# Optimization experiments

Hardware: AMD Instinct MI355X
Metric: run time of the kernel (lower is better)

The kernel has to match this reference:

```python
import jax, jax.numpy as jnp
import numpy as np

N = 50000      # num nodes
E = 1_600_000  # num edges (avg degree 32)
L = 200_000    # num label edges to decode
D_IN, H1, H2 = 256, 128, 64


def setup_inputs() -> dict:
    key = jax.random.key(0)
    ks = jax.random.split(key, 20)

    def w(k, fan_in, fan_out):
        return jax.random.normal(k, (fan_in, fan_out), jnp.float32) * (1.0 / np.sqrt(fan_in))

    return {
        'x': jax.random.normal(ks[0], (N, D_IN), jnp.float32),
        'prev0': jax.random.normal(ks[1], (N, H1), jnp.float32),
        'prev1': jax.random.normal(ks[2], (N, H2), jnp.float32),
        'Wpre1': w(ks[3], D_IN, 256), 'bpre1': jnp.zeros((256,), jnp.float32),
        'Wpre2': w(ks[4], 256, 128),  'bpre2': jnp.zeros((128,), jnp.float32),
        'Wc1': w(ks[5], 128, H1),     'bc1': jnp.zeros((H1,), jnp.float32),
        'Wc2': w(ks[6], H1, H2),      'bc2': jnp.zeros((H2,), jnp.float32),
        'Wm1': w(ks[7], 2 * H1, H1),  'bm1': jnp.zeros((H1,), jnp.float32),
        'Wm2': w(ks[8], 2 * H2, H2),  'bm2': jnp.zeros((H2,), jnp.float32),
        'Wpost': w(ks[9], H2, 2),     'bpost': jnp.zeros((2,), jnp.float32),
        'edge_index': jax.random.randint(ks[10], (2, E), 0, N, jnp.int32),
        'edge_label_index': jax.random.randint(ks[11], (2, L), 0, N, jnp.int32),
    }


def _gcn_conv(h, W, b, src, dst, n):
    """PyG GCNConv: add self-loops, sym-normalize D^-1/2 (A+I) D^-1/2 (X W) + b."""
    hw = h @ W                                   # [N, out]
    deg = jax.ops.segment_sum(jnp.ones_like(src, jnp.float32), dst, num_segments=n) + 1.0
    dinv = jax.lax.rsqrt(deg)                    # [N]
    norm = dinv[src] * dinv[dst]                 # [E]
    agg = jax.ops.segment_sum(hw[src] * norm[:, None], dst, num_segments=n)
    agg = agg + hw * (dinv * dinv)[:, None]      # self-loop term
    return agg + b


def reference(x, prev0, prev1, Wpre1, bpre1, Wpre2, bpre2, Wc1, bc1, Wc2, bc2,
              Wm1, bm1, Wm2, bm2, Wpost, bpost, edge_index, edge_label_index):
    # isnap > 0 with update='mlp'; dropout p=0.0 -> identity
    src, dst = edge_index[0], edge_index[1]
    n = x.shape[0]

    h = jax.nn.relu(x @ Wpre1 + bpre1)
    h = jax.nn.relu(h @ Wpre2 + bpre2)

    h = jax.nn.relu(_gcn_conv(h, Wc1, bc1, src, dst, n))
    h = jnp.concatenate([h, prev0], axis=1) @ Wm1 + bm1   # temporal MLP update 1
    emb0 = h

    h = jax.nn.relu(_gcn_conv(h, Wc2, bc2, src, dst, n))
    h = jnp.concatenate([h, prev1], axis=1) @ Wm2 + bm2   # temporal MLP update 2
    emb1 = h

    # hadamard edge decode
    h_had = emb1[edge_label_index[0]] * emb1[edge_label_index[1]]  # [L, H2]
    pred = jnp.sum(h_had @ Wpost + bpost, axis=-1)                 # [L]
    return pred, emb0, emb1
```

## Files before the change

### kernel.cpp

```cpp
#include <hip/hip_runtime.h>
#include <hip/hip_bf16.h>


typedef unsigned short ushort_t;
typedef __attribute__((ext_vector_type(8))) short s8v;
typedef __attribute__((ext_vector_type(4))) float f4;

#define BSHIFT 8

__device__ __forceinline__ ushort_t f2bf(float v) {
    unsigned u = __float_as_uint(v);
    return (ushort_t)((u + 0x7FFFu + ((u >> 16) & 1u)) >> 16);
}

__device__ __forceinline__ s8v cvt8(f4 v0, f4 v1) {
    ushort_t hb[8];
    hb[0] = f2bf(v0.x); hb[1] = f2bf(v0.y); hb[2] = f2bf(v0.z); hb[3] = f2bf(v0.w);
    hb[4] = f2bf(v1.x); hb[5] = f2bf(v1.y); hb[6] = f2bf(v1.z); hb[7] = f2bf(v1.w);
    return *(s8v*)hb;
}

__device__ __forceinline__ size_t swzidx(int row, int k, int Wd) {
    int p = (((k & 63) >> 3) ^ (row & 7));
    return (size_t)row * Wd + (k & ~63) + p * 8 + (k & 7);
}

__device__ __forceinline__ void dma16(const ushort_t* g, ushort_t* l) {
    __builtin_amdgcn_global_load_lds(
        (const __attribute__((address_space(1))) unsigned int*)g,
        (__attribute__((address_space(3))) unsigned int*)l, 16, 0, 0);
}

template <int W>
__global__ __launch_bounds__(256) void f2bswz_kernel(const float* __restrict__ in,
                                                     ushort_t* __restrict__ out, size_t n) {
    size_t i = ((size_t)blockIdx.x * 256 + threadIdx.x) * 8;
    if (i + 8 > n) return;
    f4 v0 = *(const f4*)&in[i];
    f4 v1 = *(const f4*)&in[i + 4];
    int row = (int)(i / W), k = (int)(i % W);
    *(s8v*)&out[swzidx(row, k, W)] = cvt8(v0, v1);
}

template <int BN, int KW, int K1, bool A1F32, bool RELU, bool SCALE, bool DUAL,
          int OUTMODE, bool SWZO>
__global__ __launch_bounds__(256, 2) void gemm_lds(
    const float* __restrict__ A1f, const ushort_t* __restrict__ A1h,
    const ushort_t* __restrict__ A2h,
    const ushort_t* __restrict__ Wt,
    const float* __restrict__ bias, const float* __restrict__ rowscale,
    float* __restrict__ Cf, ushort_t* __restrict__ Ch,
    int M, int Nout)
{
    constexpr int NT = BN / 32;
    constexpr int K2 = KW - K1;
    __shared__ ushort_t Abuf[128 * 64];
    __shared__ ushort_t Bbuf[BN * 64];

    const int tid  = threadIdx.x;
    const int lane = tid & 63;
    const int w    = tid >> 6;
    const int wr   = w >> 1, wc = w & 1;
    const int rbase = blockIdx.y * 128;
    const int bn    = blockIdx.x * BN;

    f4 acc[4][NT];
    const f4 zero = {0.f, 0.f, 0.f, 0.f};
#pragma unroll
    for (int mi = 0; mi < 4; ++mi)
#pragma unroll
        for (int ni = 0; ni < NT; ++ni) acc[mi][ni] = zero;

    for (int kt = 0; kt < KW; kt += 64) {
        if constexpr (A1F32) {
#pragma unroll
            for (int j = 0; j < 4; ++j) {
                const int c2 = tid + j * 256;
                const int row = c2 >> 3, c = c2 & 7;
                const int gr = min(rbase + row, M - 1);
                const float* p = &A1f[(size_t)gr * K1 + kt + c * 8];
                const int pc = c ^ (row & 7);
                *(s8v*)&Abuf[row * 64 + pc * 8] = cvt8(*(const f4*)p, *(const f4*)(p + 4));
            }
        } else {
#pragma unroll
            for (int i = 0; i < 4; ++i) {
                const int s = w * 4 + i;
                const int row = s * 8 + (lane >> 3);
                const int c = lane & 7;
                const int gr = min(rbase + row, M - 1);
                const ushort_t* g;
                if (DUAL && kt >= K1) g = &A2h[(size_t)gr * K2 + (kt - K1) + c * 8];
                else                  g = &A1h[(size_t)gr * K1 + kt + c * 8];
                dma16(g, &Abuf[s * 512]);
            }
        }
#pragma unroll
        for (int i = 0; i < NT; ++i) {
            const int s = w * NT + i;
            const int colr = s * 8 + (lane >> 3);
            const int c = lane & 7;
            dma16(&Wt[(size_t)(bn + colr) * KW + kt + c * 8], &Bbuf[s * 512]);
        }
        __syncthreads();
#pragma unroll
        for (int ks = 0; ks < 2; ++ks) {
            const int c = ks * 4 + (lane >> 4);
            s8v bfrag[NT];
#pragma unroll
            for (int ni = 0; ni < NT; ++ni) {
                const int colr = wc * (NT * 16) + ni * 16 + (lane & 15);
                bfrag[ni] = *(const s8v*)&Bbuf[colr * 64 + (c ^ (colr & 7)) * 8];
            }
#pragma unroll
            for (int mi = 0; mi < 4; ++mi) {
                const int row = wr * 64 + mi * 16 + (lane & 15);
                const s8v af = *(const s8v*)&Abuf[row * 64 + (c ^ (row & 7)) * 8];
#pragma unroll
                for (int ni = 0; ni < NT; ++ni)
                    acc[mi][ni] = __builtin_amdgcn_mfma_f32_16x16x32_bf16(af, bfrag[ni], acc[mi][ni], 0, 0, 0);
            }
        }
        __syncthreads();
    }

#pragma unroll
    for (int mi = 0; mi < 4; ++mi) {
#pragma unroll
        for (int reg = 0; reg < 4; ++reg) {
            const int row = rbase + wr * 64 + mi * 16 + (lane >> 4) * 4 + reg;
            if (row >= M) continue;
            const float rs = SCALE ? rowscale[row] : 1.f;
#pragma unroll
            for (int ni = 0; ni < NT; ++ni) {
                const int col = bn + wc * (NT * 16) + ni * 16 + (lane & 15);
                float v = acc[mi][ni][reg];
                if (SCALE) v *= rs;
                if (bias) v += bias[col];
                if (RELU) v = fmaxf(v, 0.f);
                const size_t oidx = SWZO ? swzidx(row, col, Nout) : ((size_t)row * Nout + col);
                if constexpr (OUTMODE == 2) {
                    Ch[oidx] = f2bf(v);
                } else if constexpr (OUTMODE == 3) {
                    Cf[(size_t)row * Nout + col] = v;
                    Ch[oidx] = f2bf(v);
                } else {
                    Cf[(size_t)row * Nout + col] = v;
                }
            }
        }
    }
}

struct WDesc { const float* W; ushort_t* h; int K; int No; };
struct WAll { WDesc d[6]; };

__global__ void wtcvt_kernel(WAll wa) {
    WDesc d = wa.d[blockIdx.y];
    int e = blockIdx.x * blockDim.x + threadIdx.x;
    if (e >= d.K * d.No) return;
    int k = e / d.No, n = e - k * d.No;
    d.h[swzidx(n, k, d.K)] = f2bf(d.W[e]);
}

__global__ __launch_bounds__(256) void bcount_kernel(const int* __restrict__ dst,
                                                     int* __restrict__ bcount, int E, int NB) {
    __shared__ int cnt[256];
    const int t = threadIdx.x;
    if (t < NB) cnt[t] = 0;
    __syncthreads();
    for (int e = blockIdx.x * 256 + t; e < E; e += gridDim.x * 256)
        atomicAdd(&cnt[dst[e] >> BSHIFT], 1);
    __syncthreads();
    if (t < NB && cnt[t]) atomicAdd(&bcount[t], cnt[t]);
}

__global__ __launch_bounds__(256) void bscan_kernel(const int* __restrict__ bcount,
                                                    int* __restrict__ bbase,
                                                    int* __restrict__ bcursor, int NB, int E) {
    __shared__ int s[256];
    const int t = threadIdx.x;
    s[t] = (t < NB) ? bcount[t] : 0;
    __syncthreads();
    for (int off = 1; off < 256; off <<= 1) {
        int v = (t >= off) ? s[t - off] : 0;
        __syncthreads();
        s[t] += v;
        __syncthreads();
    }
    int excl = t ? s[t - 1] : 0;
    if (t < NB) { bbase[t] = excl; bcursor[t] = excl; }
    if (t == 0) bbase[NB] = E;
}

__global__ __launch_bounds__(256) void bpart_kernel(const int* __restrict__ src,
                                                    const int* __restrict__ dst,
                                                    int* __restrict__ bcursor,
                                                    unsigned* __restrict__ packed, int E, int NB) {
    __shared__ int cnt[256];
    __shared__ int cur[256];
    const int t = threadIdx.x;
    const int beg = blockIdx.x * 8192;
    const int end = min(beg + 8192, E);
    if (t < NB) cnt[t] = 0;
    __syncthreads();
    for (int e = beg + t; e < end; e += 256) atomicAdd(&cnt[dst[e] >> BSHIFT], 1);
    __syncthreads();
    if (t < NB && cnt[t]) cur[t] = atomicAdd(&bcursor[t], cnt[t]);
    __syncthreads();
    for (int e = beg + t; e < end; e += 256) {
        int d = dst[e];
        int b = d >> BSHIFT;
        int pos = atomicAdd(&cur[b], 1);
        packed[pos] = (unsigned)src[e] | ((unsigned)(d & ((1 << BSHIFT) - 1)) << 16);
    }
}

__global__ __launch_bounds__(256) void bbuild_kernel(const int* __restrict__ bbase,
                                                     const unsigned* __restrict__ packed,
                                                     int* __restrict__ col,
                                                     int* __restrict__ rowstart,
                                                     float* __restrict__ dinv, int N, int E) {
    __shared__ int ncnt[256];
    __shared__ int s[256];
    __shared__ int ncur[256];
    const int b = blockIdx.x;
    const int t = threadIdx.x;
    const int beg = bbase[b], end = bbase[b + 1];
    const int node0 = b << BSHIFT;
    const int nInB = min(256, N - node0);
    ncnt[t] = 0;
    __syncthreads();
    for (int e = beg + t; e < end; e += 256) atomicAdd(&ncnt[packed[e] >> 16], 1);
    __syncthreads();
    s[t] = ncnt[t];
    __syncthreads();
    for (int off = 1; off < 256; off <<= 1) {
        int v = (t >= off) ? s[t - off] : 0;
        __syncthreads();
        s[t] += v;
        __syncthreads();
    }
    int excl = t ? s[t - 1] : 0;
    if (t < nInB) {
        rowstart[node0 + t] = beg + excl;
        dinv[node0 + t] = rsqrtf((float)ncnt[t] + 1.0f);
    }
    ncur[t] = beg + excl;
    __syncthreads();
    for (int e = beg + t; e < end; e += 256) {
        unsigned p = packed[e];
        int pos = atomicAdd(&ncur[p >> 16], 1);
        col[pos] = (int)(p & 0xFFFFu);
    }
    if (b == 0 && t == 0) rowstart[N] = E;
}

template <int F>
__global__ __launch_bounds__(256) void gather_bf_kernel(const int* __restrict__ rowstart,
                                                        const int* __restrict__ col,
                                                        const float* __restrict__ dinv,
                                                        const ushort_t* __restrict__ hws,
                                                        const float* __restrict__ bias,
                                                        ushort_t* __restrict__ aggb, int N) {
    const int wave = threadIdx.x >> 6;
    const int lane = threadIdx.x & 63;
    const int d = blockIdx.x * 4 + wave;
    if (d >= N) return;
    const int beg = rowstart[d], end = rowstart[d + 1];
    const float dd = dinv[d];
    if (F == 128) {
        const unsigned* base = (const unsigned*)hws;
        unsigned sv = base[(size_t)d * 64 + lane];
        float ax = __uint_as_float(sv << 16);
        float ay = __uint_as_float(sv & 0xFFFF0000u);
        for (int e0 = beg; e0 < end; e0 += 64) {
            int nid = (e0 + lane < end) ? col[e0 + lane] : 0;
            int cnt = min(64, end - e0);
            int j = 0;
            for (; j + 8 <= cnt; j += 8) {
                unsigned u[8];
#pragma unroll
                for (int q = 0; q < 8; ++q) {
                    int s = __shfl(nid, j + q);
                    u[q] = base[(size_t)s * 64 + lane];
                }
#pragma unroll
                for (int q = 0; q < 8; ++q) {
                    ax += __uint_as_float(u[q] << 16);
                    ay += __uint_as_float(u[q] & 0xFFFF0000u);
                }
            }
            for (; j < cnt; ++j) {
                int s = __shfl(nid, j);
                unsigned uu = base[(size_t)s * 64 + lane];
                ax += __uint_as_float(uu << 16);
                ay += __uint_as_float(uu & 0xFFFF0000u);
            }
        }
        float2 b = ((const float2*)bias)[lane];
        float rx = fmaxf(ax * dd + b.x, 0.f);
        float ry = fmaxf(ay * dd + b.y, 0.f);
        unsigned pk = ((unsigned)f2bf(ry) << 16) | (unsigned)f2bf(rx);
        const int p = ((lane >> 2) & 7) ^ (d & 7);
        const int uidx = (lane >> 5) * 32 + p * 4 + (lane & 3);
        ((unsigned*)aggb)[(size_t)d * 64 + uidx] = pk;
    } else {
        float acc = __uint_as_float((unsigned)hws[(size_t)d * 64 + lane] << 16);
        for (int e0 = beg; e0 < end; e0 += 64) {
            int nid = (e0 + lane < end) ? col[e0 + lane] : 0;
            int cnt = min(64, end - e0);
            int j = 0;
            for (; j + 8 <= cnt; j += 8) {
                ushort_t u[8];
#pragma unroll
                for (int q = 0; q < 8; ++q) {
                    int s = __shfl(nid, j + q);
                    u[q] = hws[(size_t)s * 64 + lane];
                }
#pragma unroll
                for (int q = 0; q < 8; ++q) acc += __uint_as_float((unsigned)u[q] << 16);
            }
            for (; j < cnt; ++j) {
                int s = __shfl(nid, j);
                acc += __uint_as_float((unsigned)hws[(size_t)s * 64 + lane] << 16);
            }
        }
        acc = fmaxf(acc * dd + bias[lane], 0.f);
        const int p = (lane >> 3) ^ (d & 7);
        aggb[(size_t)d * 64 + p * 8 + (lane & 7)] = f2bf(acc);
    }
}

__global__ __launch_bounds__(256) void decode_kernel(const ushort_t* __restrict__ emb1b,
                                                     const int* __restrict__ eli,
                                                     const float* __restrict__ Wpost,
                                                     const float* __restrict__ bpost,
                                                     float* __restrict__ pred, int L) {
    const int wave = threadIdx.x >> 6;
    const int lane = threadIdx.x & 63;
    const int l = blockIdx.x * 4 + wave;
    if (l >= L) return;
    int s = eli[l];
    int d = eli[L + l];
    float w = Wpost[lane * 2] + Wpost[lane * 2 + 1];
    float a = __uint_as_float((unsigned)emb1b[(size_t)s * 64 + lane] << 16);
    float b = __uint_as_float((unsigned)emb1b[(size_t)d * 64 + lane] << 16);
    float p = a * b * w;
#pragma unroll
    for (int off = 32; off; off >>= 1) p += __shfl_down(p, off);
    if (lane == 0) pred[l] = p + bpost[0] + bpost[1];
}

extern "C" void kernel_launch(void* const* d_in, const int* in_sizes, int n_in,
                              void* d_out, int out_size, void* d_ws, size_t ws_size,
                              hipStream_t stream) {
    const float* x     = (const float*)d_in[0];
    const float* prev0 = (const float*)d_in[1];
    const float* prev1 = (const float*)d_in[2];
    const float* Wpre1 = (const float*)d_in[3];
    const float* bpre1 = (const float*)d_in[4];
    const float* Wpre2 = (const float*)d_in[5];
    const float* bpre2 = (const float*)d_in[6];
    const float* Wc1   = (const float*)d_in[7];
    const float* bc1   = (const float*)d_in[8];
    const float* Wc2   = (const float*)d_in[9];
    const float* bc2   = (const float*)d_in[10];
    const float* Wm1   = (const float*)d_in[11];
    const float* bm1   = (const float*)d_in[12];
    const float* Wm2   = (const float*)d_in[13];
    const float* bm2   = (const float*)d_in[14];
    const float* Wpost = (const float*)d_in[15];
    const float* bpost = (const float*)d_in[16];
    const int* edge_index = (const int*)d_in[17];
    const int* eli        = (const int*)d_in[18];

    const int N = in_sizes[0] / 256;
    const int E = in_sizes[17] / 2;
    const int L = in_sizes[18] / 2;
    const int NB = (N + 255) >> BSHIFT;

    const int* src = edge_index;
    const int* dst = edge_index + E;

    float* out  = (float*)d_out;
    float* pred = out;
    float* emb0 = out + L;
    float* emb1 = out + L + (size_t)N * 128;

    float* ws = (float*)d_ws;
    unsigned* packed = (unsigned*)ws;
    ushort_t* h1h   = (ushort_t*)ws;
    ushort_t* hws1b = (ushort_t*)ws;
    ushort_t* emb0b = (ushort_t*)ws;
    ushort_t* emb1b = (ushort_t*)ws;
    ushort_t* agg1b = (ushort_t*)(ws + (size_t)64 * N);
    ushort_t* hws2b = (ushort_t*)(ws + (size_t)64 * N);
    ushort_t* agg2b = (ushort_t*)(ws + (size_t)96 * N);
    ushort_t* h2b   = (ushort_t*)(ws + (size_t)128 * N);
    ushort_t* p0b   = (ushort_t*)(ws + (size_t)192 * N);
    ushort_t* p1b   = (ushort_t*)(ws + (size_t)256 * N);
    int*      col   = (int*)(ws + (size_t)288 * N);

    size_t o = (size_t)320 * N;
    int* rowstart = (int*)(ws + o);         o += ((size_t)N + 4) & ~(size_t)3;
    float* dinv = ws + o;                   o += ((size_t)N + 3) & ~(size_t)3;
    int* bbase = (int*)(ws + o);            o += 260;
    int* bcursor = (int*)(ws + o);          o += 260;
    int* bcount = (int*)(ws + o);           o += 260;
    ushort_t* wb = (ushort_t*)(ws + o);

    ushort_t* wpre1t = wb + 0;
    ushort_t* wpre2t = wb + 65536;
    ushort_t* wc1t   = wb + 98304;
    ushort_t* wm1t   = wb + 114688;
    ushort_t* wc2t   = wb + 147456;
    ushort_t* wm2t   = wb + 155648;

    {
        size_t n0 = (size_t)N * 128, n1 = (size_t)N * 64;
        f2bswz_kernel<128><<<(int)((n0 / 8 + 255) / 256), 256, 0, stream>>>(prev0, p0b, n0);
        f2bswz_kernel<64><<<(int)((n1 / 8 + 255) / 256), 256, 0, stream>>>(prev1, p1b, n1);
    }

    hipMemsetAsync(bcount, 0, (size_t)NB * sizeof(int), stream);
    bcount_kernel<<<1024, 256, 0, stream>>>(dst, bcount, E, NB);
    bscan_kernel<<<1, 256, 0, stream>>>(bcount, bbase, bcursor, NB, E);
    bpart_kernel<<<(E + 8191) / 8192, 256, 0, stream>>>(src, dst, bcursor, packed, E, NB);
    bbuild_kernel<<<NB, 256, 0, stream>>>(bbase, packed, col, rowstart, dinv, N, E);

    WAll wa;
    wa.d[0] = {Wpre1, wpre1t, 256, 256};
    wa.d[1] = {Wpre2, wpre2t, 256, 128};
    wa.d[2] = {Wc1,   wc1t,   128, 128};
    wa.d[3] = {Wm1,   wm1t,   256, 128};
    wa.d[4] = {Wc2,   wc2t,   128, 64};
    wa.d[5] = {Wm2,   wm2t,   128, 64};
    wtcvt_kernel<<<dim3(256, 6), 256, 0, stream>>>(wa);

    const int gy = (N + 127) / 128;

    gemm_lds<128, 256, 256, true, true, false, false, 2, true><<<dim3(2, gy), 256, 0, stream>>>(
        x, nullptr, nullptr, wpre1t, bpre1, nullptr, nullptr, h1h, N, 256);
    gemm_lds<128, 256, 256, false, true, false, false, 2, true><<<dim3(1, gy), 256, 0, stream>>>(
        nullptr, h1h, nullptr, wpre2t, bpre2, nullptr, nullptr, h2b, N, 128);
    gemm_lds<128, 128, 128, false, false, true, false, 2, false><<<dim3(1, gy), 256, 0, stream>>>(
        nullptr, h2b, nullptr, wc1t, nullptr, dinv, nullptr, hws1b, N, 128);
    gather_bf_kernel<128><<<(N + 3) / 4, 256, 0, stream>>>(rowstart, col, dinv, hws1b, bc1, agg1b, N);
    gemm_lds<128, 256, 128, false, false, false, true, 3, true><<<dim3(1, gy), 256, 0, stream>>>(
        nullptr, agg1b, p0b, wm1t, bm1, nullptr, emb0, emb0b, N, 128);
    gemm_lds<64, 128, 128, false, false, true, false, 2, false><<<dim3(1, gy), 256, 0, stream>>>(
        nullptr, emb0b, nullptr, wc2t, nullptr, dinv, nullptr, hws2b, N, 64);
    gather_bf_kernel<64><<<(N + 3) / 4, 256, 0, stream>>>(rowstart, col, dinv, hws2b, bc2, agg2b, N);
    gemm_lds<64, 128, 64, false, false, false, true, 3, false><<<dim3(1, gy), 256, 0, stream>>>(
        nullptr, agg2b, p1b, wm2t, bm2, nullptr, emb1, emb1b, N, 64);
    decode_kernel<<<(L + 3) / 4, 256, 0, stream>>>(emb1b, eli, Wpost, bpost, pred, L);
}
```

Before: 329.0 us.

## Vectorize neighbor gather with 16-byte loads across lane groups and batch decode

The GCN aggregation kernels now split each wave into lane groups that each load a full neighbor row segment with 16-byte uint4 loads. This processes 4 (F=128) or 8 (F=64) neighbors in parallel per iteration, and the partial sums are reduced with cross-lane shuffles. The decode kernel similarly handles 8 label edges per wave using 16-byte row loads. The aim is to cut the count of narrow memory instructions and raise memory-level parallelism, at the cost of masked idle lanes on ragged tails and extra shuffle reductions.

Measured after the change: 301.0 us. -8.5%, faster.

```diff
diff --git a/kernel.cpp b/kernel.cpp
--- a/kernel.cpp
+++ b/kernel.cpp
@@ -29,6 +29,17 @@
     __builtin_amdgcn_global_load_lds(
         (const __attribute__((address_space(1))) unsigned int*)g,
         (__attribute__((address_space(3))) unsigned int*)l, 16, 0, 0);
+}
+
+__device__ __forceinline__ void add8(float* acc, uint4 u, float m) {
+    acc[0] = fmaf(__uint_as_float(u.x << 16), m, acc[0]);
+    acc[1] = fmaf(__uint_as_float(u.x & 0xFFFF0000u), m, acc[1]);
+    acc[2] = fmaf(__uint_as_float(u.y << 16), m, acc[2]);
+    acc[3] = fmaf(__uint_as_float(u.y & 0xFFFF0000u), m, acc[3]);
+    acc[4] = fmaf(__uint_as_float(u.z << 16), m, acc[4]);
+    acc[5] = fmaf(__uint_as_float(u.z & 0xFFFF0000u), m, acc[5]);
+    acc[6] = fmaf(__uint_as_float(u.w << 16), m, acc[6]);
+    acc[7] = fmaf(__uint_as_float(u.w & 0xFFFF0000u), m, acc[7]);
 }
 
 template <int W>
@@ -257,99 +268,133 @@
 }
 
 template <int F>
-__global__ __launch_bounds__(256) void gather_bf_kernel(const int* __restrict__ rowstart,
-                                                        const int* __restrict__ col,
-                                                        const float* __restrict__ dinv,
-                                                        const ushort_t* __restrict__ hws,
-                                                        const float* __restrict__ bias,
-                                                        ushort_t* __restrict__ aggb, int N) {
+__global__ __launch_bounds__(256) void gather4_kernel(const int* __restrict__ rowstart,
+                                                      const int* __restrict__ col,
+                                                      const float* __restrict__ dinv,
+                                                      const ushort_t* __restrict__ hws,
+                                                      const float* __restrict__ bias,
+                                                      ushort_t* __restrict__ aggb, int N) {
     const int wave = threadIdx.x >> 6;
     const int lane = threadIdx.x & 63;
     const int d = blockIdx.x * 4 + wave;
     if (d >= N) return;
     const int beg = rowstart[d], end = rowstart[d + 1];
     const float dd = dinv[d];
+    const uint4* rowp = (const uint4*)hws;
+
     if (F == 128) {
-        const unsigned* base = (const unsigned*)hws;
-        unsigned sv = base[(size_t)d * 64 + lane];
-        float ax = __uint_as_float(sv << 16);
-        float ay = __uint_as_float(sv & 0xFFFF0000u);
+        const int q = lane >> 4;
+        const int c = lane & 15;
+        float acc[8] = {};
+        uint4 sv = rowp[(size_t)d * 16 + c];
+        if (q == 0) add8(acc, sv, 1.f);
         for (int e0 = beg; e0 < end; e0 += 64) {
             int nid = (e0 + lane < end) ? col[e0 + lane] : 0;
             int cnt = min(64, end - e0);
-            int j = 0;
-            for (; j + 8 <= cnt; j += 8) {
-                unsigned u[8];
-#pragma unroll
-                for (int q = 0; q < 8; ++q) {
-                    int s = __shfl(nid, j + q);
-                    u[q] = base[(size_t)s * 64 + lane];
-                }
-#pragma unroll
-                for (int q = 0; q < 8; ++q) {
-                    ax += __uint_as_float(u[q] << 16);
-                    ay += __uint_as_float(u[q] & 0xFFFF0000u);
-                }
-            }
-            for (; j < cnt; ++j) {
-                int s = __shfl(nid, j);
-                unsigned uu = base[(size_t)s * 64 + lane];
-                ax += __uint_as_float(uu << 16);
-                ay += __uint_as_float(uu & 0xFFFF0000u);
-            }
-        }
-        float2 b = ((const float2*)bias)[lane];
-        float rx = fmaxf(ax * dd + b.x, 0.f);
-        float ry = fmaxf(ay * dd + b.y, 0.f);
-        unsigned pk = ((unsigned)f2bf(ry) << 16) | (unsigned)f2bf(rx);
-        const int p = ((lane >> 2) & 7) ^ (d & 7);
-        const int uidx = (lane >> 5) * 32 + p * 4 + (lane & 3);
-        ((unsigned*)aggb)[(size_t)d * 64 + uidx] = pk;
+            for (int jj = 0; jj < cnt; jj += 4) {
+                int s = __shfl(nid, jj + q);
+                float m = (jj + q < cnt) ? 1.f : 0.f;
+                uint4 u = rowp[(size_t)s * 16 + c];
+                add8(acc, u, m);
+            }
+        }
+#pragma unroll
+        for (int i = 0; i < 8; ++i) {
+            acc[i] += __shfl_down(acc[i], 32);
+            acc[i] += __shfl_down(acc[i], 16);
+        }
+        if (q == 0) {
+            f4 b0 = *(const f4*)&bias[c * 8];
+            f4 b1 = *(const f4*)&bias[c * 8 + 4];
+            float r[8];
+            r[0] = fmaxf(acc[0] * dd + b0.x, 0.f); r[1] = fmaxf(acc[1] * dd + b0.y, 0.f);
+            r[2] = fmaxf(acc[2] * dd + b0.z, 0.f); r[3] = fmaxf(acc[3] * dd + b0.w, 0.f);
+            r[4] = fmaxf(acc[4] * dd + b1.x, 0.f); r[5] = fmaxf(acc[5] * dd + b1.y, 0.f);
+            r[6] = fmaxf(acc[6] * dd + b1.z, 0.f); r[7] = fmaxf(acc[7] * dd + b1.w, 0.f);
+            uint4 o;
+            o.x = (unsigned)f2bf(r[0]) | ((unsigned)f2bf(r[1]) << 16);
+            o.y = (unsigned)f2bf(r[2]) | ((unsigned)f2bf(r[3]) << 16);
+            o.z = (unsigned)f2bf(r[4]) | ((unsigned)f2bf(r[5]) << 16);
+            o.w = (unsigned)f2bf(r[6]) | ((unsigned)f2bf(r[7]) << 16);
+            const int g = c >> 3;
+            const int ch = (c & 7) ^ (d & 7);
+            ((uint4*)aggb)[(size_t)d * 16 + g * 8 + ch] = o;
+        }
     } else {
-        float acc = __uint_as_float((unsigned)hws[(size_t)d * 64 + lane] << 16);
+        const int q = lane >> 3;
+        const int c = lane & 7;
+        float acc[8] = {};
+        uint4 sv = rowp[(size_t)d * 8 + c];
+        if (q == 0) add8(acc, sv, 1.f);
         for (int e0 = beg; e0 < end; e0 += 64) {
             int nid = (e0 + lane < end) ? col[e0 + lane] : 0;
             int cnt = min(64, end - e0);
-            int j = 0;
-            for (; j + 8 <= cnt; j += 8) {
-                ushort_t u[8];
-#pragma unroll
-                for (int q = 0; q < 8; ++q) {
-                    int s = __shfl(nid, j + q);
-                    u[q] = hws[(size_t)s * 64 + lane];
-                }
-#pragma unroll
-                for (int q = 0; q < 8; ++q) acc += __uint_as_float((unsigned)u[q] << 16);
-            }
-            for (; j < cnt; ++j) {
-                int s = __shfl(nid, j);
-                acc += __uint_as_float((unsigned)hws[(size_t)s * 64 + lane] << 16);
-            }
-        }
-        acc = fmaxf(acc * dd + bias[lane], 0.f);
-        const int p = (lane >> 3) ^ (d & 7);
-        aggb[(size_t)d * 64 + p * 8 + (lane & 7)] = f2bf(acc);
-    }
-}
-
-__global__ __launch_bounds__(256) void decode_kernel(const ushort_t* __restrict__ emb1b,
-                                                     const int* __restrict__ eli,
-                                                     const float* __restrict__ Wpost,
-                                                     const float* __restrict__ bpost,
-                                                     float* __restrict__ pred, int L) {
+            for (int jj = 0; jj < cnt; jj += 8) {
+                int s = __shfl(nid, jj + q);
+                float m = (jj + q < cnt) ? 1.f : 0.f;
+                uint4 u = rowp[(size_t)s * 8 + c];
+                add8(acc, u, m);
+            }
+        }
+#pragma unroll
+        for (int i = 0; i < 8; ++i) {
+            acc[i] += __shfl_down(acc[i], 32);
+            acc[i] += __shfl_down(acc[i], 16);
+            acc[i] += __shfl_down(acc[i], 8);
+        }
+        if (q == 0) {
+            f4 b0 = *(const f4*)&bias[c * 8];
+            f4 b1 = *(const f4*)&bias[c * 8 + 4];
+            float r[8];
+            r[0] = fmaxf(acc[0] * dd + b0.x, 0.f); r[1] = fmaxf(acc[1] * dd + b0.y, 0.f);
+            r[2] = fmaxf(acc[2] * dd + b0.z, 0.f); r[3] = fmaxf(acc[3] * dd + b0.w, 0.f);
+            r[4] = fmaxf(acc[4] * dd + b1.x, 0.f); r[5] = fmaxf(acc[5] * dd + b1.y, 0.f);
+            r[6] = fmaxf(acc[6] * dd + b1.z, 0.f); r[7] = fmaxf(acc[7] * dd + b1.w, 0.f);
+            uint4 o;
+            o.x = (unsigned)f2bf(r[0]) | ((unsigned)f2bf(r[1]) << 16);
+            o.y = (unsigned)f2bf(r[2]) | ((unsigned)f2bf(r[3]) << 16);
+            o.z = (unsigned)f2bf(r[4]) | ((unsigned)f2bf(r[5]) << 16);
+            o.w = (unsigned)f2bf(r[6]) | ((unsigned)f2bf(r[7]) << 16);
+            const int ch = c ^ (d & 7);
+            ((uint4*)aggb)[(size_t)d * 8 + ch] = o;
+        }
+    }
+}
+
+__global__ __launch_bounds__(256) void decode8_kernel(const ushort_t* __restrict__ emb1b,
+                                                      const int* __restrict__ eli,
+                                                      const float* __restrict__ Wpost,
+                                                      const float* __restrict__ bpost,
+                                                      float* __restrict__ pred, int L) {
     const int wave = threadIdx.x >> 6;
     const int lane = threadIdx.x & 63;
-    const int l = blockIdx.x * 4 + wave;
-    if (l >= L) return;
-    int s = eli[l];
-    int d = eli[L + l];
-    float w = Wpost[lane * 2] + Wpost[lane * 2 + 1];
-    float a = __uint_as_float((unsigned)emb1b[(size_t)s * 64 + lane] << 16);
-    float b = __uint_as_float((unsigned)emb1b[(size_t)d * 64 + lane] << 16);
-    float p = a * b * w;
-#pragma unroll
-    for (int off = 32; off; off >>= 1) p += __shfl_down(p, off);
-    if (lane == 0) pred[l] = p + bpost[0] + bpost[1];
+    const int l8 = (blockIdx.x * 4 + wave) * 8;
+    if (l8 >= L) return;
+    const int q = lane >> 3;
+    const int c = lane & 7;
+    const int l = min(l8 + q, L - 1);
+    const int s = eli[l];
+    const int d = eli[L + l];
+    const uint4* rowp = (const uint4*)emb1b;
+    uint4 ua = rowp[(size_t)s * 8 + c];
+    uint4 ub = rowp[(size_t)d * 8 + c];
+    f4 w0 = *(const f4*)&Wpost[c * 16];
+    f4 w1 = *(const f4*)&Wpost[c * 16 + 4];
+    f4 w2 = *(const f4*)&Wpost[c * 16 + 8];
+    f4 w3 = *(const f4*)&Wpost[c * 16 + 12];
+    float p = 0.f;
+    p += __uint_as_float(ua.x << 16) * __uint_as_float(ub.x << 16) * (w0.x + w0.y);
+    p += __uint_as_float(ua.x & 0xFFFF0000u) * __uint_as_float(ub.x & 0xFFFF0000u) * (w0.z + w0.w);
+    p += __uint_as_float(ua.y << 16) * __uint_as_float(ub.y << 16) * (w1.x + w1.y);
+    p += __uint_as_float(ua.y & 0xFFFF0000u) * __uint_as_float(ub.y & 0xFFFF0000u) * (w1.z + w1.w);
+    p += __uint_as_float(ua.z << 16) * __uint_as_float(ub.z << 16) * (w2.x + w2.y);
+    p += __uint_as_float(ua.z & 0xFFFF0000u) * __uint_as_float(ub.z & 0xFFFF0000u) * (w2.z + w2.w);
+    p += __uint_as_float(ua.w << 16) * __uint_as_float(ub.w << 16) * (w3.x + w3.y);
+    p += __uint_as_float(ua.w & 0xFFFF0000u) * __uint_as_float(ub.w & 0xFFFF0000u) * (w3.z + w3.w);
+    p += __shfl_down(p, 4);
+    p += __shfl_down(p, 2);
+    p += __shfl_down(p, 1);
+    if (c == 0 && l8 + q < L) pred[l8 + q] = p + bpost[0] + bpost[1];
 }
 
 extern "C" void kernel_launch(void* const* d_in, const int* in_sizes, int n_in,
@@ -446,13 +491,13 @@
         nullptr, h1h, nullptr, wpre2t, bpre2, nullptr, nullptr, h2b, N, 128);
     gemm_lds<128, 128, 128, false, false, true, false, 2, false><<<dim3(1, gy), 256, 0, stream>>>(
         nullptr, h2b, nullptr, wc1t, nullptr, dinv, nullptr, hws1b, N, 128);
-    gather_bf_kernel<128><<<(N + 3) / 4, 256, 0, stream>>>(rowstart, col, dinv, hws1b, bc1, agg1b, N);
+    gather4_kernel<128><<<(N + 3) / 4, 256, 0, stream>>>(rowstart, col, dinv, hws1b, bc1, agg1b, N);
     gemm_lds<128, 256, 128, false, false, false, true, 3, true><<<dim3(1, gy), 256, 0, stream>>>(
         nullptr, agg1b, p0b, wm1t, bm1, nullptr, emb0, emb0b, N, 128);
     gemm_lds<64, 128, 128, false, false, true, false, 2, false><<<dim3(1, gy), 256, 0, stream>>>(
         nullptr, emb0b, nullptr, wc2t, nullptr, dinv, nullptr, hws2b, N, 64);
-    gather_bf_kernel<64><<<(N + 3) / 4, 256, 0, stream>>>(rowstart, col, dinv, hws2b, bc2, agg2b, N);
+    gather4_kernel<64><<<(N + 3) / 4, 256, 0, stream>>>(rowstart, col, dinv, hws2b, bc2, agg2b, N);
     gemm_lds<64, 128, 64, false, false, false, true, 3, false><<<dim3(1, gy), 256, 0, stream>>>(
         nullptr, agg2b, p1b, wm2t, bm2, nullptr, emb1, emb1b, N, 64);
-    decode_kernel<<<(L + 3) / 4, 256, 0, stream>>>(emb1b, eli, Wpost, bpost, pred, L);
-}
+    decode8_kernel<<<(L + 31) / 32, 256, 0, stream>>>(emb1b, eli, Wpost, bpost, pred, L);
+}
```
